# Kernel optimization log

Measured on AMD Instinct MI355X. Metric: run time of the kernel, lower is better.

The kernel has to match this reference:

```python
import jax, jax.numpy as jnp
import numpy as np


def setup_inputs() -> dict:
    key = jax.random.key(0)
    ks = jax.random.split(key, 6)
    B, H, W, C = 8, 128, 128, 256
    x = jax.random.normal(ks[0], (B, H, W), dtype=jnp.float32)
    atten_x_full = jax.random.normal(ks[1], (B, H, W, W), dtype=jnp.float32)
    atten_y_full = jax.random.normal(ks[2], (B, W, H, H), dtype=jnp.float32)
    value_full = jax.random.normal(ks[3], (B, H, W, C), dtype=jnp.float32)
    # nn.Parameter init: shift = |randn|, bias = -|randn|
    shift = jnp.abs(jax.random.normal(ks[4], (1,), dtype=jnp.float32))
    bias = -jnp.abs(jax.random.normal(ks[5], (1,), dtype=jnp.float32))
    return {"x": x, "atten_x_full": atten_x_full, "atten_y_full": atten_y_full,
            "value_full": value_full, "shift": shift, "bias": bias}


def reference(x, atten_x_full, atten_y_full, value_full, shift, bias):
    H, W = x.shape[1], x.shape[2]
    # Gaussian distance biases: gx[c, h] = -(shift*(h-c)^2 + bias), gy[r, w] likewise
    hw = jnp.arange(W, dtype=jnp.float32)
    hh = jnp.arange(H, dtype=jnp.float32)
    gx = -(shift[0] * (hw[None, :] - hw[:, None]) ** 2 + bias[0])  # [W, W]
    gy = -(shift[0] * (hh[None, :] - hh[:, None]) ** 2 + bias[0])  # [H, H]
    # atten_x_full indexed [b, r, c, k] -> add gx[c, k]; softmax over k (row direction)
    Ax = jax.nn.softmax(atten_x_full + gx[None, None, :, :], axis=-1)  # [B,H,W,W]
    # atten_y_full indexed [b, c, r, k] -> add gy[r, k]; softmax over k (col direction)
    Ay = jax.nn.softmax(atten_y_full + gy[None, None, :, :], axis=-1)  # [B,W,H,H]
    out = (jnp.einsum('brck,brkd->brcd', Ax, value_full)
           + jnp.einsum('bcrk,bkcd->brcd', Ay, value_full))  # [B,H,W,C]
    return out
```

## Files before the change

kernel.cpp:

```cpp
#include <hip/hip_runtime.h>

typedef __attribute__((ext_vector_type(8))) short short8;
typedef __attribute__((ext_vector_type(4))) float floatx4;

#define LDK 136
#define LDS_BYTES (256 * LDK * 2)

__device__ __forceinline__ unsigned f2bf1(float x) {
    unsigned u = __builtin_bit_cast(unsigned, x);
    return (u + 0x7fffu + ((u >> 16) & 1u)) >> 16;
}
__device__ __forceinline__ unsigned packbf(float lo, float hi) {
    return f2bf1(lo) | (f2bf1(hi) << 16);
}

template <bool ACCUM>
__global__ __launch_bounds__(512, 4) void gtrans(
    const float* __restrict__ atten, const float* __restrict__ value,
    float* __restrict__ out, const float* __restrict__ shiftp,
    const float* __restrict__ biasp, int s0, int s1)
{
    extern __shared__ short Buf[];
    unsigned* Buf32 = (unsigned*)Buf;

    const int bi   = blockIdx.x;
    const int b    = bi >> 7;
    const int i    = bi & 127;
    const int tid  = threadIdx.x;
    const int lane = tid & 63;
    const int w    = tid >> 6;

    const float shift = shiftp[0];
    const float bias  = biasp[0];

    const float* abase = atten + (size_t)bi * (128 * 128);
    const float* vbase = value + (size_t)b * (128 * 128 * 256) + (size_t)i * s0;
    float*       obase = out   + (size_t)b * (128 * 128 * 256) + (size_t)i * s0;

    const int rrow = 16 * w + (lane & 15);
    const int kq8  = (lane >> 4) * 8;
    const int k0   = 16 * w + 2 * (lane >> 3);
    const int d0   = 4 * (lane & 7);

    floatx4 aA[8];
#pragma unroll
    for (int ks = 0; ks < 4; ++ks) {
        const float* ap = abase + rrow * 128 + ks * 32 + kq8;
        aA[2 * ks]     = *(const floatx4*)(ap);
        aA[2 * ks + 1] = *(const floatx4*)(ap + 4);
    }
    floatx4 va[8], vb[8];
    {
        const float* vp0 = vbase + (size_t)k0 * s1 + d0;
        const float* vp1 = vp0 + s1;
#pragma unroll
        for (int q = 0; q < 8; ++q) va[q] = *(const floatx4*)(vp0 + 32 * q);
#pragma unroll
        for (int q = 0; q < 8; ++q) vb[q] = *(const floatx4*)(vp1 + 32 * q);
    }
    __builtin_amdgcn_sched_barrier(0);

    floatx4 e8[8];
    {
        float mx = -1e30f;
#pragma unroll
        for (int j = 0; j < 8; ++j) {
            const int kb = (j >> 1) * 32 + kq8 + (j & 1) * 4;
            floatx4 v = aA[j];
            floatx4 t;
#pragma unroll
            for (int e = 0; e < 4; ++e) {
                float d = (float)(kb + e - rrow);
                t[e] = v[e] - (shift * d * d + bias);
            }
            e8[j] = t;
            mx = fmaxf(mx, fmaxf(fmaxf(t[0], t[1]), fmaxf(t[2], t[3])));
        }
        mx = fmaxf(mx, __shfl_xor(mx, 16, 64));
        mx = fmaxf(mx, __shfl_xor(mx, 32, 64));
        float ssum = 0.0f;
#pragma unroll
        for (int j = 0; j < 8; ++j) {
            floatx4 t = e8[j];
#pragma unroll
            for (int e = 0; e < 4; ++e) t[e] = __expf(t[e] - mx);
            e8[j] = t;
            ssum += (t[0] + t[1]) + (t[2] + t[3]);
        }
        ssum += __shfl_xor(ssum, 16, 64);
        ssum += __shfl_xor(ssum, 32, 64);
        float r = 1.0f / ssum;
#pragma unroll
        for (int j = 0; j < 8; ++j) {
#pragma unroll
            for (int e = 0; e < 4; ++e) e8[j][e] *= r;
        }
    }

    short8 bfrag[4];
#pragma unroll
    for (int ks = 0; ks < 4; ++ks) {
        union { short8 s; unsigned u[4]; } uu;
        floatx4 lo = e8[2 * ks], hi = e8[2 * ks + 1];
        uu.u[0] = packbf(lo[0], lo[1]);
        uu.u[1] = packbf(lo[2], lo[3]);
        uu.u[2] = packbf(hi[0], hi[1]);
        uu.u[3] = packbf(hi[2], hi[3]);
        bfrag[ks] = uu.s;
    }

#pragma unroll
    for (int q = 0; q < 8; ++q)
#pragma unroll
        for (int e = 0; e < 4; ++e)
            Buf32[(d0 + 32 * q + e) * (LDK / 2) + (k0 >> 1)] = packbf(va[q][e], vb[q][e]);

    const int dq = 4 * (lane >> 4);
    float* orow = obase + (size_t)rrow * s1 + dq;
    floatx4 aO[4];
    if (ACCUM) {
#pragma unroll
        for (int t = 0; t < 4; ++t) aO[t] = *(const floatx4*)(orow + t * 16);
    }

    __builtin_amdgcn_sched_barrier(0);
    asm volatile("s_waitcnt lgkmcnt(0)" ::: "memory");
    __builtin_amdgcn_s_barrier();

#pragma unroll
    for (int g = 0; g < 4; ++g) {
        floatx4 aN[4];
        if (ACCUM && g < 3) {
#pragma unroll
            for (int t = 0; t < 4; ++t)
                aN[t] = *(const floatx4*)(orow + (g + 1) * 64 + t * 16);
        }
        floatx4 acc[4];
#pragma unroll
        for (int t = 0; t < 4; ++t) acc[t] = (floatx4)0.0f;
#pragma unroll
        for (int tt = 0; tt < 4; ++tt) {
            const short* base = &Buf[((g * 4 + tt) * 16 + (lane & 15)) * LDK + kq8];
#pragma unroll
            for (int ks = 0; ks < 4; ++ks) {
                short8 af = *(const short8*)(base + ks * 32);
                acc[tt] = __builtin_amdgcn_mfma_f32_16x16x32_bf16(af, bfrag[ks], acc[tt], 0, 0, 0);
            }
        }
#pragma unroll
        for (int t = 0; t < 4; ++t) {
            floatx4 res = acc[t];
            if (ACCUM) res = res + aO[t];
            *(floatx4*)(orow + g * 64 + t * 16) = res;
        }
        if (ACCUM && g < 3) {
#pragma unroll
            for (int t = 0; t < 4; ++t) aO[t] = aN[t];
        }
    }
}

extern "C" void kernel_launch(void* const* d_in, const int* in_sizes, int n_in,
                              void* d_out, int out_size, void* d_ws, size_t ws_size,
                              hipStream_t stream) {
    const float* atten_x = (const float*)d_in[1];
    const float* atten_y = (const float*)d_in[2];
    const float* value   = (const float*)d_in[3];
    const float* shiftp  = (const float*)d_in[4];
    const float* biasp   = (const float*)d_in[5];
    float* out = (float*)d_out;

    static bool inited = false;
    if (!inited) {
        hipFuncSetAttribute((const void*)&gtrans<false>,
                            hipFuncAttributeMaxDynamicSharedMemorySize, LDS_BYTES);
        hipFuncSetAttribute((const void*)&gtrans<true>,
                            hipFuncAttributeMaxDynamicSharedMemorySize, LDS_BYTES);
        inited = true;
    }

    dim3 grid(1024), block(512);
    gtrans<false><<<grid, block, LDS_BYTES, stream>>>(atten_x, value, out, shiftp, biasp,
                                                      128 * 256, 256);
    gtrans<true><<<grid, block, LDS_BYTES, stream>>>(atten_y, value, out, shiftp, biasp,
                                                     256, 128 * 256);
}
```

Measured before the change: 409.4 us.

## Process two tiles per block and prefetch next value tile during MFMA

```diff
diff --git a/kernel.cpp b/kernel.cpp
--- a/kernel.cpp
+++ b/kernel.cpp
@@ -14,6 +14,10 @@
     return f2bf1(lo) | (f2bf1(hi) << 16);
 }
 
+#define VL(reg, p, o) \
+    asm volatile("global_load_dwordx4 %0, %1, off offset:" o \
+                 : "=v"(reg) : "v"(p) : "memory")
+
 template <bool ACCUM>
 __global__ __launch_bounds__(512, 4) void gtrans(
     const float* __restrict__ atten, const float* __restrict__ value,
@@ -23,9 +27,6 @@
     extern __shared__ short Buf[];
     unsigned* Buf32 = (unsigned*)Buf;
 
-    const int bi   = blockIdx.x;
-    const int b    = bi >> 7;
-    const int i    = bi & 127;
     const int tid  = threadIdx.x;
     const int lane = tid & 63;
     const int w    = tid >> 6;
@@ -33,41 +34,44 @@
     const float shift = shiftp[0];
     const float bias  = biasp[0];
 
-    const float* abase = atten + (size_t)bi * (128 * 128);
-    const float* vbase = value + (size_t)b * (128 * 128 * 256) + (size_t)i * s0;
-    float*       obase = out   + (size_t)b * (128 * 128 * 256) + (size_t)i * s0;
-
     const int rrow = 16 * w + (lane & 15);
     const int kq8  = (lane >> 4) * 8;
     const int k0   = 16 * w + 2 * (lane >> 3);
     const int d0   = 4 * (lane & 7);
+    const int am   = lane & 15;
+    const int dq   = 4 * (lane >> 4);
 
-    floatx4 aA[8];
+    floatx4 va[8], vb[8];
+    short8 bfrag[4];
+
+    auto issueV = [&](int ti) {
+        const int b = ti >> 7, i = ti & 127;
+        const float* vp0 = value + (size_t)b * (128 * 128 * 256) + (size_t)i * s0
+                         + (size_t)k0 * s1 + d0;
+        const float* vp1 = vp0 + s1;
+        VL(va[0], vp0, "0");   VL(va[1], vp0, "128"); VL(va[2], vp0, "256");
+        VL(va[3], vp0, "384"); VL(va[4], vp0, "512"); VL(va[5], vp0, "640");
+        VL(va[6], vp0, "768"); VL(va[7], vp0, "896");
+        VL(vb[0], vp1, "0");   VL(vb[1], vp1, "128"); VL(vb[2], vp1, "256");
+        VL(vb[3], vp1, "384"); VL(vb[4], vp1, "512"); VL(vb[5], vp1, "640");
+        VL(vb[6], vp1, "768"); VL(vb[7], vp1, "896");
+    };
+
+    auto softmax_bfrag = [&](int ti) {
+        const float* abase = atten + (size_t)ti * (128 * 128);
+        floatx4 aA[8];
 #pragma unroll
-    for (int ks = 0; ks < 4; ++ks) {
-        const float* ap = abase + rrow * 128 + ks * 32 + kq8;
-        aA[2 * ks]     = *(const floatx4*)(ap);
-        aA[2 * ks + 1] = *(const floatx4*)(ap + 4);
-    }
-    floatx4 va[8], vb[8];
-    {
-        const float* vp0 = vbase + (size_t)k0 * s1 + d0;
-        const float* vp1 = vp0 + s1;
-#pragma unroll
-        for (int q = 0; q < 8; ++q) va[q] = *(const floatx4*)(vp0 + 32 * q);
-#pragma unroll
-        for (int q = 0; q < 8; ++q) vb[q] = *(const floatx4*)(vp1 + 32 * q);
-    }
-    __builtin_amdgcn_sched_barrier(0);
-
-    floatx4 e8[8];
-    {
+        for (int ks = 0; ks < 4; ++ks) {
+            const float* ap = abase + rrow * 128 + ks * 32 + kq8;
+            aA[2 * ks]     = *(const floatx4*)(ap);
+            aA[2 * ks + 1] = *(const floatx4*)(ap + 4);
+        }
+        floatx4 e8[8];
         float mx = -1e30f;
 #pragma unroll
         for (int j = 0; j < 8; ++j) {
             const int kb = (j >> 1) * 32 + kq8 + (j & 1) * 4;
-            floatx4 v = aA[j];
-            floatx4 t;
+            floatx4 v = aA[j], t;
 #pragma unroll
             for (int e = 0; e < 4; ++e) {
                 float d = (float)(kb + e - rrow);
@@ -91,73 +95,80 @@
         ssum += __shfl_xor(ssum, 32, 64);
         float r = 1.0f / ssum;
 #pragma unroll
-        for (int j = 0; j < 8; ++j) {
+        for (int ks = 0; ks < 4; ++ks) {
+            union { short8 s; unsigned u[4]; } uu;
+            floatx4 lo = e8[2 * ks], hi = e8[2 * ks + 1];
+            uu.u[0] = packbf(lo[0] * r, lo[1] * r);
+            uu.u[1] = packbf(lo[2] * r, lo[3] * r);
+            uu.u[2] = packbf(hi[0] * r, hi[1] * r);
+            uu.u[3] = packbf(hi[2] * r, hi[3] * r);
+            bfrag[ks] = uu.s;
+        }
+    };
+
+    auto stage = [&]() {
 #pragma unroll
-            for (int e = 0; e < 4; ++e) e8[j][e] *= r;
+        for (int q = 0; q < 8; ++q)
+#pragma unroll
+            for (int e = 0; e < 4; ++e)
+                Buf32[(d0 + 32 * q + e) * (LDK / 2) + (k0 >> 1)] = packbf(va[q][e], vb[q][e]);
+    };
+
+    auto mfma_phase = [&](int ti) {
+        const int b = ti >> 7, i = ti & 127;
+        float* orow = out + (size_t)b * (128 * 128 * 256) + (size_t)i * s0
+                    + (size_t)rrow * s1 + dq;
+#pragma unroll
+        for (int g = 0; g < 4; ++g) {
+            floatx4 acc[4];
+            if (ACCUM) {
+#pragma unroll
+                for (int t = 0; t < 4; ++t)
+                    acc[t] = *(const floatx4*)(orow + g * 64 + t * 16);
+            } else {
+#pragma unroll
+                for (int t = 0; t < 4; ++t) acc[t] = (floatx4)0.0f;
+            }
+#pragma unroll
+            for (int tt = 0; tt < 4; ++tt) {
+                const short* base = &Buf[((g * 4 + tt) * 16 + am) * LDK + kq8];
+#pragma unroll
+                for (int ks = 0; ks < 4; ++ks) {
+                    short8 af = *(const short8*)(base + ks * 32);
+                    acc[tt] = __builtin_amdgcn_mfma_f32_16x16x32_bf16(af, bfrag[ks], acc[tt], 0, 0, 0);
+                }
+            }
+#pragma unroll
+            for (int t = 0; t < 4; ++t)
+                *(floatx4*)(orow + g * 64 + t * 16) = acc[t];
         }
-    }
+    };
 
-    short8 bfrag[4];
-#pragma unroll
-    for (int ks = 0; ks < 4; ++ks) {
-        union { short8 s; unsigned u[4]; } uu;
-        floatx4 lo = e8[2 * ks], hi = e8[2 * ks + 1];
-        uu.u[0] = packbf(lo[0], lo[1]);
-        uu.u[1] = packbf(lo[2], lo[3]);
-        uu.u[2] = packbf(hi[0], hi[1]);
-        uu.u[3] = packbf(hi[2], hi[3]);
-        bfrag[ks] = uu.s;
-    }
+    const int ti0 = blockIdx.x;
+    const int ti1 = blockIdx.x + 512;
 
-#pragma unroll
-    for (int q = 0; q < 8; ++q)
-#pragma unroll
-        for (int e = 0; e < 4; ++e)
-            Buf32[(d0 + 32 * q + e) * (LDK / 2) + (k0 >> 1)] = packbf(va[q][e], vb[q][e]);
+    issueV(ti0);
+    softmax_bfrag(ti0);
+    __builtin_amdgcn_sched_barrier(0);
+    asm volatile("s_waitcnt vmcnt(0)" ::: "memory");
+    __builtin_amdgcn_sched_barrier(0);
+    stage();
+    __builtin_amdgcn_sched_barrier(0);
+    asm volatile("s_waitcnt lgkmcnt(0)" ::: "memory");
+    issueV(ti1);
+    __builtin_amdgcn_s_barrier();
+    mfma_phase(ti0);
+    __builtin_amdgcn_s_barrier();
 
-    const int dq = 4 * (lane >> 4);
-    float* orow = obase + (size_t)rrow * s1 + dq;
-    floatx4 aO[4];
-    if (ACCUM) {
-#pragma unroll
-        for (int t = 0; t < 4; ++t) aO[t] = *(const floatx4*)(orow + t * 16);
-    }
-
+    softmax_bfrag(ti1);
+    __builtin_amdgcn_sched_barrier(0);
+    asm volatile("s_waitcnt vmcnt(0)" ::: "memory");
+    __builtin_amdgcn_sched_barrier(0);
+    stage();
     __builtin_amdgcn_sched_barrier(0);
     asm volatile("s_waitcnt lgkmcnt(0)" ::: "memory");
     __builtin_amdgcn_s_barrier();
-
-#pragma unroll
-    for (int g = 0; g < 4; ++g) {
-        floatx4 aN[4];
-        if (ACCUM && g < 3) {
-#pragma unroll
-            for (int t = 0; t < 4; ++t)
-                aN[t] = *(const floatx4*)(orow + (g + 1) * 64 + t * 16);
-        }
-        floatx4 acc[4];
-#pragma unroll
-        for (int t = 0; t < 4; ++t) acc[t] = (floatx4)0.0f;
-#pragma unroll
-        for (int tt = 0; tt < 4; ++tt) {
-            const short* base = &Buf[((g * 4 + tt) * 16 + (lane & 15)) * LDK + kq8];
-#pragma unroll
-            for (int ks = 0; ks < 4; ++ks) {
-                short8 af = *(const short8*)(base + ks * 32);
-                acc[tt] = __builtin_amdgcn_mfma_f32_16x16x32_bf16(af, bfrag[ks], acc[tt], 0, 0, 0);
-            }
-        }
-#pragma unroll
-        for (int t = 0; t < 4; ++t) {
-            floatx4 res = acc[t];
-            if (ACCUM) res = res + aO[t];
-            *(floatx4*)(orow + g * 64 + t * 16) = res;
-        }
-        if (ACCUM && g < 3) {
-#pragma unroll
-            for (int t = 0; t < 4; ++t) aO[t] = aN[t];
-        }
-    }
+    mfma_phase(ti1);
 }
 
 extern "C" void kernel_launch(void* const* d_in, const int* in_sizes, int n_in,
@@ -179,7 +190,7 @@
         inited = true;
     }
 
-    dim3 grid(1024), block(512);
+    dim3 grid(512), block(512);
     gtrans<false><<<grid, block, LDS_BYTES, stream>>>(atten_x, value, out, shiftp, biasp,
                                                       128 * 256, 256);
     gtrans<true><<<grid, block, LDS_BYTES, stream>>>(atten_y, value, out, shiftp, biasp,
```

New measurement: 450.1 us. +9.9%, slower.

## Store first-pass partial output as fp16 in workspace and accumulate into MMA

Applied to the files above, without the earlier changes.

```diff
diff --git a/kernel.cpp b/kernel.cpp
--- a/kernel.cpp
+++ b/kernel.cpp
@@ -2,9 +2,11 @@
 
 typedef __attribute__((ext_vector_type(8))) short short8;
 typedef __attribute__((ext_vector_type(4))) float floatx4;
+typedef _Float16 half4 __attribute__((ext_vector_type(4)));
 
 #define LDK 136
 #define LDS_BYTES (256 * LDK * 2)
+#define OUT_ELEMS (8LL * 128 * 128 * 256)
 
 __device__ __forceinline__ unsigned f2bf1(float x) {
     unsigned u = __builtin_bit_cast(unsigned, x);
@@ -14,11 +16,12 @@
     return f2bf1(lo) | (f2bf1(hi) << 16);
 }
 
-template <bool ACCUM>
+template <int MODE>
 __global__ __launch_bounds__(512, 4) void gtrans(
     const float* __restrict__ atten, const float* __restrict__ value,
-    float* __restrict__ out, const float* __restrict__ shiftp,
-    const float* __restrict__ biasp, int s0, int s1)
+    float* __restrict__ out, _Float16* __restrict__ ws,
+    const float* __restrict__ shiftp, const float* __restrict__ biasp,
+    int s0, int s1)
 {
     extern __shared__ short Buf[];
     unsigned* Buf32 = (unsigned*)Buf;
@@ -33,21 +36,23 @@
     const float shift = shiftp[0];
     const float bias  = biasp[0];
 
+    const size_t obase_off = (size_t)b * (128 * 128 * 256) + (size_t)i * s0;
     const float* abase = atten + (size_t)bi * (128 * 128);
-    const float* vbase = value + (size_t)b * (128 * 128 * 256) + (size_t)i * s0;
-    float*       obase = out   + (size_t)b * (128 * 128 * 256) + (size_t)i * s0;
+    const float* vbase = value + obase_off;
 
     const int rrow = 16 * w + (lane & 15);
     const int kq8  = (lane >> 4) * 8;
     const int k0   = 16 * w + 2 * (lane >> 3);
     const int d0   = 4 * (lane & 7);
+    const int am   = lane & 15;
+    const int dq   = 4 * (lane >> 4);
 
     floatx4 aA[8];
 #pragma unroll
     for (int ks = 0; ks < 4; ++ks) {
         const float* ap = abase + rrow * 128 + ks * 32 + kq8;
-        aA[2 * ks]     = *(const floatx4*)(ap);
-        aA[2 * ks + 1] = *(const floatx4*)(ap + 4);
+        aA[2 * ks]     = __builtin_nontemporal_load((const floatx4*)(ap));
+        aA[2 * ks + 1] = __builtin_nontemporal_load((const floatx4*)(ap + 4));
     }
     floatx4 va[8], vb[8];
     {
@@ -58,16 +63,15 @@
 #pragma unroll
         for (int q = 0; q < 8; ++q) vb[q] = *(const floatx4*)(vp1 + 32 * q);
     }
-    __builtin_amdgcn_sched_barrier(0);
-
-    floatx4 e8[8];
+
+    short8 bfrag[4];
     {
+        floatx4 e8[8];
         float mx = -1e30f;
 #pragma unroll
         for (int j = 0; j < 8; ++j) {
             const int kb = (j >> 1) * 32 + kq8 + (j & 1) * 4;
-            floatx4 v = aA[j];
-            floatx4 t;
+            floatx4 v = aA[j], t;
 #pragma unroll
             for (int e = 0; e < 4; ++e) {
                 float d = (float)(kb + e - rrow);
@@ -91,22 +95,15 @@
         ssum += __shfl_xor(ssum, 32, 64);
         float r = 1.0f / ssum;
 #pragma unroll
-        for (int j = 0; j < 8; ++j) {
-#pragma unroll
-            for (int e = 0; e < 4; ++e) e8[j][e] *= r;
-        }
-    }
-
-    short8 bfrag[4];
-#pragma unroll
-    for (int ks = 0; ks < 4; ++ks) {
-        union { short8 s; unsigned u[4]; } uu;
-        floatx4 lo = e8[2 * ks], hi = e8[2 * ks + 1];
-        uu.u[0] = packbf(lo[0], lo[1]);
-        uu.u[1] = packbf(lo[2], lo[3]);
-        uu.u[2] = packbf(hi[0], hi[1]);
-        uu.u[3] = packbf(hi[2], hi[3]);
-        bfrag[ks] = uu.s;
+        for (int ks = 0; ks < 4; ++ks) {
+            union { short8 s; unsigned u[4]; } uu;
+            floatx4 lo = e8[2 * ks], hi = e8[2 * ks + 1];
+            uu.u[0] = packbf(lo[0] * r, lo[1] * r);
+            uu.u[1] = packbf(lo[2] * r, lo[3] * r);
+            uu.u[2] = packbf(hi[0] * r, hi[1] * r);
+            uu.u[3] = packbf(hi[2] * r, hi[3] * r);
+            bfrag[ks] = uu.s;
+        }
     }
 
 #pragma unroll
@@ -114,33 +111,36 @@
 #pragma unroll
         for (int e = 0; e < 4; ++e)
             Buf32[(d0 + 32 * q + e) * (LDK / 2) + (k0 >> 1)] = packbf(va[q][e], vb[q][e]);
-
-    const int dq = 4 * (lane >> 4);
-    float* orow = obase + (size_t)rrow * s1 + dq;
-    floatx4 aO[4];
-    if (ACCUM) {
-#pragma unroll
-        for (int t = 0; t < 4; ++t) aO[t] = *(const floatx4*)(orow + t * 16);
-    }
 
     __builtin_amdgcn_sched_barrier(0);
     asm volatile("s_waitcnt lgkmcnt(0)" ::: "memory");
     __builtin_amdgcn_s_barrier();
 
+    float*     orow = out + obase_off + (size_t)rrow * s1 + dq;
+    _Float16*  wrow = ws  + obase_off + (size_t)rrow * s1 + dq;
 #pragma unroll
     for (int g = 0; g < 4; ++g) {
-        floatx4 aN[4];
-        if (ACCUM && g < 3) {
+        floatx4 acc[4];
+        if (MODE == 2) {
 #pragma unroll
             for (int t = 0; t < 4; ++t)
-                aN[t] = *(const floatx4*)(orow + (g + 1) * 64 + t * 16);
-        }
-        floatx4 acc[4];
-#pragma unroll
-        for (int t = 0; t < 4; ++t) acc[t] = (floatx4)0.0f;
+                acc[t] = *(const floatx4*)(orow + g * 64 + t * 16);
+        } else if (MODE == 3) {
+#pragma unroll
+            for (int t = 0; t < 4; ++t) {
+                half4 h = *(const half4*)(wrow + g * 64 + t * 16);
+                floatx4 f;
+#pragma unroll
+                for (int e = 0; e < 4; ++e) f[e] = (float)h[e];
+                acc[t] = f;
+            }
+        } else {
+#pragma unroll
+            for (int t = 0; t < 4; ++t) acc[t] = (floatx4)0.0f;
+        }
 #pragma unroll
         for (int tt = 0; tt < 4; ++tt) {
-            const short* base = &Buf[((g * 4 + tt) * 16 + (lane & 15)) * LDK + kq8];
+            const short* base = &Buf[((g * 4 + tt) * 16 + am) * LDK + kq8];
 #pragma unroll
             for (int ks = 0; ks < 4; ++ks) {
                 short8 af = *(const short8*)(base + ks * 32);
@@ -149,13 +149,16 @@
         }
 #pragma unroll
         for (int t = 0; t < 4; ++t) {
-            floatx4 res = acc[t];
-            if (ACCUM) res = res + aO[t];
-            *(floatx4*)(orow + g * 64 + t * 16) = res;
-        }
-        if (ACCUM && g < 3) {
-#pragma unroll
-            for (int t = 0; t < 4; ++t) aO[t] = aN[t];
+            if (MODE == 1) {
+                half4 h;
+#pragma unroll
+                for (int e = 0; e < 4; ++e) h[e] = (_Float16)acc[t][e];
+                *(half4*)(wrow + g * 64 + t * 16) = h;
+            } else if (MODE == 3) {
+                __builtin_nontemporal_store(acc[t], (floatx4*)(orow + g * 64 + t * 16));
+            } else {
+                *(floatx4*)(orow + g * 64 + t * 16) = acc[t];
+            }
         }
     }
 }
@@ -169,19 +172,29 @@
     const float* shiftp  = (const float*)d_in[4];
     const float* biasp   = (const float*)d_in[5];
     float* out = (float*)d_out;
+    _Float16* ws = (_Float16*)d_ws;
 
     static bool inited = false;
     if (!inited) {
-        hipFuncSetAttribute((const void*)&gtrans<false>,
-                            hipFuncAttributeMaxDynamicSharedMemorySize, LDS_BYTES);
-        hipFuncSetAttribute((const void*)&gtrans<true>,
-                            hipFuncAttributeMaxDynamicSharedMemorySize, LDS_BYTES);
+        hipFuncSetAttribute((const void*)&gtrans<0>, hipFuncAttributeMaxDynamicSharedMemorySize, LDS_BYTES);
+        hipFuncSetAttribute((const void*)&gtrans<1>, hipFuncAttributeMaxDynamicSharedMemorySize, LDS_BYTES);
+        hipFuncSetAttribute((const void*)&gtrans<2>, hipFuncAttributeMaxDynamicSharedMemorySize, LDS_BYTES);
+        hipFuncSetAttribute((const void*)&gtrans<3>, hipFuncAttributeMaxDynamicSharedMemorySize, LDS_BYTES);
         inited = true;
     }
 
+    const bool use_ws = (ws != nullptr) && (ws_size >= (size_t)OUT_ELEMS * sizeof(_Float16));
+
     dim3 grid(1024), block(512);
-    gtrans<false><<<grid, block, LDS_BYTES, stream>>>(atten_x, value, out, shiftp, biasp,
+    if (use_ws) {
+        gtrans<1><<<grid, block, LDS_BYTES, stream>>>(atten_x, value, out, ws, shiftp, biasp,
                                                       128 * 256, 256);
-    gtrans<true><<<grid, block, LDS_BYTES, stream>>>(atten_y, value, out, shiftp, biasp,
-                                                     256, 128 * 256);
-}
+        gtrans<3><<<grid, block, LDS_BYTES, stream>>>(atten_y, value, out, ws, shiftp, biasp,
+                                                      256, 128 * 256);
+    } else {
+        gtrans<0><<<grid, block, LDS_BYTES, stream>>>(atten_x, value, out, ws, shiftp, biasp,
+                                                      128 * 256, 256);
+        gtrans<2><<<grid, block, LDS_BYTES, stream>>>(atten_y, value, out, ws, shiftp, biasp,
+                                                      256, 128 * 256);
+    }
+}
```

Result: faster. 365.4 us (-10.8%).
